# Optimization experiments

Measured on AMD Instinct MI355X. Metric: run time of the kernel, lower is better.

Reference implementation:

```python
import jax, jax.numpy as jnp
import numpy as np

N_NODES = 100000


def gcn_conv(x, W, b, row, col, ew, n_nodes):
    """PyG GCNConv: add self-loops (weight 1), symmetric normalization,
    out[c] = sum_{(r,c) in E} norm * (x @ W)[r] + b."""
    sl = jnp.arange(n_nodes, dtype=row.dtype)
    row2 = jnp.concatenate([row, sl])
    col2 = jnp.concatenate([col, sl])
    ew2 = jnp.concatenate([ew, jnp.ones((n_nodes,), dtype=ew.dtype)])
    deg = jax.ops.segment_sum(ew2, col2, num_segments=n_nodes)  # [N]
    dinv = jnp.where(deg > 0, jax.lax.rsqrt(jnp.where(deg > 0, deg, 1.0)), 0.0)
    norm = dinv[row2] * ew2 * dinv[col2]                         # [E+N]
    h = x @ W                                                    # [N, out]
    msg = h[row2] * norm[:, None]                                # gather + scale
    out = jax.ops.segment_sum(msg, col2, num_segments=n_nodes)   # scatter-add
    return out + b


def setup_inputs() -> dict:
    key = jax.random.key(0)
    k1, k2, k3, k4, k5 = jax.random.split(key, 5)
    F_IN, HID, C = 512, 16, 40
    E = 3200000
    x = jax.random.normal(k1, (N_NODES, F_IN), dtype=jnp.float32)
    edge_index = jax.random.randint(k2, (2, E), 0, N_NODES, dtype=jnp.int64)
    edge_weight = jax.random.uniform(k3, (E,), dtype=jnp.float32)
    # Glorot-ish init for weights
    W1 = jax.random.normal(k4, (F_IN, HID), dtype=jnp.float32) / np.sqrt(F_IN)
    b1 = jnp.zeros((HID,), dtype=jnp.float32)
    W2 = jax.random.normal(k5, (HID, C), dtype=jnp.float32) / np.sqrt(HID)
    b2 = jnp.zeros((C,), dtype=jnp.float32)
    return {"x": x, "edge_index": edge_index, "edge_weight": edge_weight,
            "W1": W1, "b1": b1, "W2": W2, "b2": b2}


def reference(x, edge_index, edge_weight, W1, b1, W2, b2):
    row, col = edge_index[0], edge_index[1]
    h = jax.nn.relu(gcn_conv(x, W1, b1, row, col, edge_weight, N_NODES))
    # dropout p=0.1 is identity at inference; DFALayer/DFA are identity in forward
    logits = gcn_conv(h, W2, b2, row, col, edge_weight, N_NODES)
    return jax.nn.log_softmax(logits, axis=1)
```

## Files before the change

kernel.cpp:

```cpp
#include <hip/hip_runtime.h>
#include <hip/hip_bf16.h>
#include <math.h>

#define F_IN 512
#define HID  16
#define C_OUT 40

#define BSH    7
#define BNODES 128
#define MAXNB  1024

#define EPB 8192
#define CTH 512

__device__ __forceinline__ unsigned short f2bf(float f) {
    unsigned u = __float_as_uint(f);
    unsigned r = (u + 0x7FFF + ((u >> 16) & 1)) >> 16;
    return (unsigned short)r;
}
__device__ __forceinline__ float bf2f(unsigned short h) {
    return __uint_as_float(((unsigned)h) << 16);
}

__global__ __launch_bounds__(1024) void k_zero(int* __restrict__ g, int n) {
    int t = threadIdx.x;
    if (t < n) g[t] = 0;
}

__global__ __launch_bounds__(CTH) void k_count(const int* __restrict__ col,
                                               int* __restrict__ gcnt,
                                               int E, int NB) {
    __shared__ int lc[MAXNB];
    int t = threadIdx.x;
    for (int i = t; i < NB; i += CTH) lc[i] = 0;
    __syncthreads();
    int base = blockIdx.x * EPB;
#pragma unroll
    for (int i = 0; i < EPB / CTH; ++i) {
        int e = base + t + i * CTH;
        if (e < E) atomicAdd(&lc[col[e] >> BSH], 1);
    }
    __syncthreads();
    for (int i = t; i < NB; i += CTH)
        if (lc[i]) atomicAdd(&gcnt[i], lc[i]);
}

__global__ __launch_bounds__(1024) void k_scan(const int* __restrict__ gcnt,
                                               int* __restrict__ bo,
                                               int* __restrict__ bcur,
                                               int* __restrict__ offs,
                                               int NB, int N, int E) {
    __shared__ int s[1024];
    int t = threadIdx.x;
    int v = (t < NB) ? gcnt[t] : 0;
    s[t] = v;
    __syncthreads();
    for (int off = 1; off < 1024; off <<= 1) {
        int x = (t >= off) ? s[t - off] : 0;
        __syncthreads();
        s[t] += x;
        __syncthreads();
    }
    if (t < NB) { int o = s[t] - v; bo[t] = o; bcur[t] = o; }
    if (t == 0) { bo[NB] = E; offs[N] = E; }
}

__global__ __launch_bounds__(CTH) void k_part(const int* __restrict__ row,
                                              const int* __restrict__ col,
                                              const float* __restrict__ ew,
                                              int* __restrict__ bcur,
                                              int2* __restrict__ st,
                                              int E, int NB) {
    __shared__ int lc[MAXNB];
    __shared__ int lb[MAXNB];
    int t = threadIdx.x;
    for (int i = t; i < NB; i += CTH) lc[i] = 0;
    __syncthreads();
    int base = blockIdx.x * EPB;
#pragma unroll
    for (int i = 0; i < EPB / CTH; ++i) {
        int e = base + t + i * CTH;
        if (e < E) atomicAdd(&lc[col[e] >> BSH], 1);
    }
    __syncthreads();
    for (int i = t; i < NB; i += CTH) {
        int c = lc[i];
        lb[i] = c ? atomicAdd(&bcur[i], c) : 0;
    }
    __syncthreads();
    for (int i = t; i < NB; i += CTH) lc[i] = 0;
    __syncthreads();
#pragma unroll
    for (int i = 0; i < EPB / CTH; ++i) {
        int e = base + t + i * CTH;
        if (e < E) {
            int c = col[e];
            int b = c >> BSH;
            int r = atomicAdd(&lc[b], 1);
            st[lb[b] + r] = make_int2((row[e] << BSH) | (c & (BNODES - 1)),
                                      __float_as_int(ew[e]));
        }
    }
}

__global__ __launch_bounds__(256) void k_sort(const int* __restrict__ bo,
                                              const int2* __restrict__ st,
                                              int2* __restrict__ st2,
                                              int* __restrict__ offs,
                                              float* __restrict__ dinv, int N) {
    __shared__ int cnt[BNODES];
    __shared__ float wsum[BNODES];
    __shared__ int off[BNODES];
    int t = threadIdx.x;
    int b = blockIdx.x;
    if (t < BNODES) { cnt[t] = 0; wsum[t] = 0.0f; }
    __syncthreads();
    int beg = bo[b], end = bo[b + 1];
    for (int e = beg + t; e < end; e += 256) {
        int2 rec = st[e];
        int cl = rec.x & (BNODES - 1);
        atomicAdd(&cnt[cl], 1);
        atomicAdd(&wsum[cl], __int_as_float(rec.y));
    }
    __syncthreads();
    if (t < BNODES) off[t] = cnt[t];
    __syncthreads();
    for (int o = 1; o < BNODES; o <<= 1) {
        int v = (t < BNODES && t >= o) ? off[t - o] : 0;
        __syncthreads();
        if (t < BNODES) off[t] += v;
        __syncthreads();
    }
    if (t < BNODES) {
        int ex = off[t] - cnt[t];
        off[t] = ex;
        int n = b * BNODES + t;
        if (n < N) {
            offs[n] = beg + ex;
            dinv[n] = rsqrtf(1.0f + wsum[t]);
        }
        cnt[t] = 0;
    }
    __syncthreads();
    for (int e = beg + t; e < end; e += 256) {
        int2 rec = st[e];
        int cl = rec.x & (BNODES - 1);
        int r = atomicAdd(&cnt[cl], 1);
        st2[beg + off[cl] + r] = make_int2(rec.x >> BSH, rec.y);
    }
}

__global__ __launch_bounds__(256) void k_gemm1(const float* __restrict__ x,
                                               const float* __restrict__ W,
                                               const float* __restrict__ dinv,
                                               unsigned short* __restrict__ hb,
                                               int N) {
    int n = blockIdx.x * 256 + threadIdx.x;
    if (n >= N) return;
    float acc[HID];
#pragma unroll
    for (int j = 0; j < HID; ++j) acc[j] = 0.0f;
    const float4* xr = (const float4*)(x + (size_t)n * F_IN);
#pragma unroll 4
    for (int k4 = 0; k4 < F_IN / 4; ++k4) {
        float4 xv = xr[k4];
        const float* wk = W + k4 * 4 * HID;
#pragma unroll
        for (int j = 0; j < HID; ++j) acc[j] += xv.x * wk[j];
#pragma unroll
        for (int j = 0; j < HID; ++j) acc[j] += xv.y * wk[HID + j];
#pragma unroll
        for (int j = 0; j < HID; ++j) acc[j] += xv.z * wk[2 * HID + j];
#pragma unroll
        for (int j = 0; j < HID; ++j) acc[j] += xv.w * wk[3 * HID + j];
    }
    float d = dinv[n];
    unsigned pk[8];
#pragma unroll
    for (int j = 0; j < 8; ++j)
        pk[j] = (unsigned)f2bf(d * acc[2 * j]) |
                ((unsigned)f2bf(d * acc[2 * j + 1]) << 16);
    uint4* hp = (uint4*)(hb + (size_t)n * HID);
    hp[0] = make_uint4(pk[0], pk[1], pk[2], pk[3]);
    hp[1] = make_uint4(pk[4], pk[5], pk[6], pk[7]);
}

__global__ __launch_bounds__(256) void k_agg1(const int* __restrict__ offs,
                                              const int2* __restrict__ st2,
                                              const float* __restrict__ dinv,
                                              const unsigned short* __restrict__ srcb,
                                              const float* __restrict__ bias,
                                              unsigned short* __restrict__ dstb,
                                              int N) {
    int t = threadIdx.x;
    int lane = t & 63, w = t >> 6;
    int n = blockIdx.x * 4 + w;
    if (n >= N) return;
    int q = lane & 3, i = lane >> 2;
    int beg = offs[n], end = offs[n + 1];
    float4 acc = make_float4(0.f, 0.f, 0.f, 0.f);
    for (int e = beg + i; e < end; e += 16) {
        int2 rec = st2[e];
        float wt = __int_as_float(rec.y);
        ushort4 v = ((const ushort4*)(srcb + (size_t)rec.x * HID))[q];
        acc.x += wt * bf2f(v.x);
        acc.y += wt * bf2f(v.y);
        acc.z += wt * bf2f(v.z);
        acc.w += wt * bf2f(v.w);
    }
#pragma unroll
    for (int off = 4; off < 64; off <<= 1) {
        acc.x += __shfl_xor(acc.x, off, 64);
        acc.y += __shfl_xor(acc.y, off, 64);
        acc.z += __shfl_xor(acc.z, off, 64);
        acc.w += __shfl_xor(acc.w, off, 64);
    }
    if (i == 0) {
        float d = dinv[n];
        ushort4 sv = ((const ushort4*)(srcb + (size_t)n * HID))[q];
        float4 bq = ((const float4*)bias)[q];
        float r0 = d * fmaxf(d * (acc.x + bf2f(sv.x)) + bq.x, 0.f);
        float r1 = d * fmaxf(d * (acc.y + bf2f(sv.y)) + bq.y, 0.f);
        float r2 = d * fmaxf(d * (acc.z + bf2f(sv.z)) + bq.z, 0.f);
        float r3 = d * fmaxf(d * (acc.w + bf2f(sv.w)) + bq.w, 0.f);
        ((ushort4*)(dstb + (size_t)n * HID))[q] =
            make_ushort4(f2bf(r0), f2bf(r1), f2bf(r2), f2bf(r3));
    }
}

__global__ __launch_bounds__(256) void k_agg2(const int* __restrict__ offs,
                                              const int2* __restrict__ st2,
                                              const float* __restrict__ dinv,
                                              const unsigned short* __restrict__ srcb,
                                              const float* __restrict__ W2,
                                              const float* __restrict__ b2,
                                              float* __restrict__ out, int N) {
    __shared__ float Ws[HID * C_OUT];
    __shared__ float bs[C_OUT];
    int t = threadIdx.x;
    for (int iw = t; iw < HID * C_OUT; iw += 256) Ws[iw] = W2[iw];
    if (t < C_OUT) bs[t] = b2[t];
    __syncthreads();

    int lane = t & 63, w = t >> 6;
    int n = blockIdx.x * 4 + w;
    if (n >= N) return;
    int q = lane & 3, i = lane >> 2;
    int beg = offs[n], end = offs[n + 1];
    float4 acc = make_float4(0.f, 0.f, 0.f, 0.f);
    for (int e = beg + i; e < end; e += 16) {
        int2 rec = st2[e];
        float wt = __int_as_float(rec.y);
        ushort4 v = ((const ushort4*)(srcb + (size_t)rec.x * HID))[q];
        acc.x += wt * bf2f(v.x);
        acc.y += wt * bf2f(v.y);
        acc.z += wt * bf2f(v.z);
        acc.w += wt * bf2f(v.w);
    }
#pragma unroll
    for (int off = 4; off < 64; off <<= 1) {
        acc.x += __shfl_xor(acc.x, off, 64);
        acc.y += __shfl_xor(acc.y, off, 64);
        acc.z += __shfl_xor(acc.z, off, 64);
        acc.w += __shfl_xor(acc.w, off, 64);
    }
    float d = dinv[n];
    ushort4 sv = ((const ushort4*)(srcb + (size_t)n * HID))[q];
    float gq[4];
    gq[0] = d * (acc.x + bf2f(sv.x));
    gq[1] = d * (acc.y + bf2f(sv.y));
    gq[2] = d * (acc.z + bf2f(sv.z));
    gq[3] = d * (acc.w + bf2f(sv.w));
    float g16[16];
    int base = lane & ~3;
#pragma unroll
    for (int qq = 0; qq < 4; ++qq) {
#pragma unroll
        for (int k = 0; k < 4; ++k)
            g16[qq * 4 + k] = __shfl(gq[k], base + qq, 64);
    }
    float logit = -INFINITY;
    if (lane < C_OUT) {
        float a = bs[lane];
#pragma unroll
        for (int j = 0; j < HID; ++j) a += g16[j] * Ws[j * C_OUT + lane];
        logit = a;
    }
    float m = logit;
#pragma unroll
    for (int off = 32; off > 0; off >>= 1) m = fmaxf(m, __shfl_xor(m, off, 64));
    float ex = (lane < C_OUT) ? __expf(logit - m) : 0.0f;
    float s = ex;
#pragma unroll
    for (int off = 32; off > 0; off >>= 1) s += __shfl_xor(s, off, 64);
    if (lane < C_OUT) out[(size_t)n * C_OUT + lane] = logit - m - __logf(s);
}

extern "C" void kernel_launch(void* const* d_in, const int* in_sizes, int n_in,
                              void* d_out, int out_size, void* d_ws, size_t ws_size,
                              hipStream_t stream) {
    const float* x   = (const float*)d_in[0];
    const int*   ei  = (const int*)d_in[1];
    const float* ew  = (const float*)d_in[2];
    const float* W1  = (const float*)d_in[3];
    const float* b1  = (const float*)d_in[4];
    const float* W2  = (const float*)d_in[5];
    const float* b2  = (const float*)d_in[6];
    float* out = (float*)d_out;

    const int N = in_sizes[0] / F_IN;
    const int E = in_sizes[2];
    const int* row = ei;
    const int* col = ei + E;
    const int NB = (N + BNODES - 1) >> BSH;

    int* wsi = (int*)d_ws;
    size_t o = 0;
    int* gcnt  = wsi + o; o += MAXNB;
    int* bo    = wsi + o; o += MAXNB + 1;
    int* bcur  = wsi + o; o += MAXNB;
    int* offs  = wsi + o; o += (size_t)N + 8;
    float* dinv = (float*)(wsi + o); o += N;
    unsigned short* h1b = (unsigned short*)(wsi + o); o += (size_t)N * HID / 2;
    unsigned short* a1b = (unsigned short*)(wsi + o); o += (size_t)N * HID / 2;
    int2* st   = (int2*)(wsi + o); o += (size_t)E * 2;
    int2* st2  = (int2*)(wsi + o); o += (size_t)E * 2;

    int gC = (E + EPB - 1) / EPB;
    int gW = (N + 3) / 4;

    k_zero<<<1, 1024, 0, stream>>>(gcnt, NB);
    k_count<<<gC, CTH, 0, stream>>>(col, gcnt, E, NB);
    k_scan<<<1, 1024, 0, stream>>>(gcnt, bo, bcur, offs, NB, N, E);
    k_part<<<gC, CTH, 0, stream>>>(row, col, ew, bcur, st, E, NB);
    k_sort<<<NB, 256, 0, stream>>>(bo, st, st2, offs, dinv, N);
    k_gemm1<<<(N + 255) / 256, 256, 0, stream>>>(x, W1, dinv, h1b, N);
    k_agg1<<<gW, 256, 0, stream>>>(offs, st2, dinv, h1b, b1, a1b, N);
    k_agg2<<<gW, 256, 0, stream>>>(offs, st2, dinv, a1b, W2, b2, out, N);
}
```

Before: 629.8 us.

## Stage x tiles into LDS via async global_load_lds with double buffering in gemm1

The first GEMM kernel no longer has each thread read its own 2KB row of x with strided float4 loads. It now cooperatively streams 32-column tiles of 256 rows into LDS using the direct global-to-LDS load builtin, with two buffers and an XOR swizzle to avoid bank conflicts. The aim is coalesced global reads of x (about 200MB, which dominates this kernel) and overlap of the next tile's load with the FMA work. The cost is 64KB of LDS per block, which limits occupancy, plus a barrier per tile.

```diff
diff --git a/kernel.cpp b/kernel.cpp
--- a/kernel.cpp
+++ b/kernel.cpp
@@ -12,6 +12,9 @@
 
 #define EPB 8192
 #define CTH 512
+
+#define GTK 32
+#define GTILES (F_IN / GTK)
 
 __device__ __forceinline__ unsigned short f2bf(float f) {
     unsigned u = __float_as_uint(f);
@@ -20,6 +23,12 @@
 }
 __device__ __forceinline__ float bf2f(unsigned short h) {
     return __uint_as_float(((unsigned)h) << 16);
+}
+
+__device__ __forceinline__ void gll16(const float* gp, void* lp) {
+    __builtin_amdgcn_global_load_lds(
+        (const __attribute__((address_space(1))) void*)gp,
+        (__attribute__((address_space(3))) void*)lp, 16, 0, 0);
 }
 
 __global__ __launch_bounds__(1024) void k_zero(int* __restrict__ g, int n) {
@@ -155,25 +164,58 @@
                                                const float* __restrict__ dinv,
                                                unsigned short* __restrict__ hb,
                                                int N) {
-    int n = blockIdx.x * 256 + threadIdx.x;
+    __shared__ float4 xt[2][256][8];
+
+    const int t = threadIdx.x;
+    const int lane = t & 63;
+    const int w = t >> 6;
+    const int lr = lane >> 3;
+    const int sc = (lane & 7) ^ lr;
+    const int n0 = blockIdx.x * 256;
+
+#define STAGE(kt, b)                                                        \
+    {                                                                       \
+        _Pragma("unroll")                                                   \
+        for (int it = 0; it < 8; ++it) {                                    \
+            int q  = w * 8 + it;              \
+            int rr = n0 + q * 8 + lr;                                       \
+            if (rr >= N) rr = N - 1;                                        \
+            const float* gp = x + (size_t)rr * F_IN + (kt) * GTK + sc * 4;  \
+            gll16(gp, (void*)&xt[b][q * 8][0]);                             \
+        }                                                                   \
+    }
+
+    float acc[HID];
+#pragma unroll
+    for (int j = 0; j < HID; ++j) acc[j] = 0.0f;
+
+    STAGE(0, 0);
+    __syncthreads();
+
+    const int sw = t & 7;
+    for (int kt = 0; kt < GTILES; ++kt) {
+        int b = kt & 1;
+        if (kt + 1 < GTILES) STAGE(kt + 1, b ^ 1);
+        const float4* xrow = &xt[b][t][0];
+#pragma unroll
+        for (int c = 0; c < 8; ++c) {
+            float4 xv = xrow[c ^ sw];
+            const float* wk = W + ((kt * GTK) + c * 4) * HID;
+#pragma unroll
+            for (int j = 0; j < HID; ++j) acc[j] += xv.x * wk[j];
+#pragma unroll
+            for (int j = 0; j < HID; ++j) acc[j] += xv.y * wk[HID + j];
+#pragma unroll
+            for (int j = 0; j < HID; ++j) acc[j] += xv.z * wk[2 * HID + j];
+#pragma unroll
+            for (int j = 0; j < HID; ++j) acc[j] += xv.w * wk[3 * HID + j];
+        }
+        __syncthreads();
+    }
+#undef STAGE
+
+    int n = n0 + t;
     if (n >= N) return;
-    float acc[HID];
-#pragma unroll
-    for (int j = 0; j < HID; ++j) acc[j] = 0.0f;
-    const float4* xr = (const float4*)(x + (size_t)n * F_IN);
-#pragma unroll 4
-    for (int k4 = 0; k4 < F_IN / 4; ++k4) {
-        float4 xv = xr[k4];
-        const float* wk = W + k4 * 4 * HID;
-#pragma unroll
-        for (int j = 0; j < HID; ++j) acc[j] += xv.x * wk[j];
-#pragma unroll
-        for (int j = 0; j < HID; ++j) acc[j] += xv.y * wk[HID + j];
-#pragma unroll
-        for (int j = 0; j < HID; ++j) acc[j] += xv.z * wk[2 * HID + j];
-#pragma unroll
-        for (int j = 0; j < HID; ++j) acc[j] += xv.w * wk[3 * HID + j];
-    }
     float d = dinv[n];
     unsigned pk[8];
 #pragma unroll
```

New measurement: 677.1 us. 7.5% more time.

## Restructure x@W1 GEMM to wave-per-row-block with coalesced loads and shuffle reduction

Applied to the files above, without the earlier changes.

The first-layer GEMM previously had each thread compute one full row, so each thread read a 2KB row with a large stride across the wave. Now each wave processes 16 rows: every lane holds a slice of W1 in registers, reads a coalesced float4 pair of each x row, prefetches the next row, and reduces the 16 outputs across lanes with a butterfly transpose-reduce via xor shuffles. This targets the uncoalesced, bandwidth-heavy x reads (about 200MB) at the cost of heavy register use (launch bounds 256,1), many shuffles per row, and fewer blocks in flight.

```diff
diff --git a/kernel.cpp b/kernel.cpp
--- a/kernel.cpp
+++ b/kernel.cpp
@@ -150,39 +150,115 @@
     }
 }
 
-__global__ __launch_bounds__(256) void k_gemm1(const float* __restrict__ x,
-                                               const float* __restrict__ W,
-                                               const float* __restrict__ dinv,
-                                               unsigned short* __restrict__ hb,
-                                               int N) {
-    int n = blockIdx.x * 256 + threadIdx.x;
-    if (n >= N) return;
-    float acc[HID];
-#pragma unroll
-    for (int j = 0; j < HID; ++j) acc[j] = 0.0f;
-    const float4* xr = (const float4*)(x + (size_t)n * F_IN);
-#pragma unroll 4
-    for (int k4 = 0; k4 < F_IN / 4; ++k4) {
-        float4 xv = xr[k4];
-        const float* wk = W + k4 * 4 * HID;
-#pragma unroll
-        for (int j = 0; j < HID; ++j) acc[j] += xv.x * wk[j];
-#pragma unroll
-        for (int j = 0; j < HID; ++j) acc[j] += xv.y * wk[HID + j];
-#pragma unroll
-        for (int j = 0; j < HID; ++j) acc[j] += xv.z * wk[2 * HID + j];
-#pragma unroll
-        for (int j = 0; j < HID; ++j) acc[j] += xv.w * wk[3 * HID + j];
-    }
-    float d = dinv[n];
-    unsigned pk[8];
-#pragma unroll
-    for (int j = 0; j < 8; ++j)
-        pk[j] = (unsigned)f2bf(d * acc[2 * j]) |
-                ((unsigned)f2bf(d * acc[2 * j + 1]) << 16);
-    uint4* hp = (uint4*)(hb + (size_t)n * HID);
-    hp[0] = make_uint4(pk[0], pk[1], pk[2], pk[3]);
-    hp[1] = make_uint4(pk[4], pk[5], pk[6], pk[7]);
+#define ROWS_PER_WAVE 16
+
+__global__ __launch_bounds__(256, 1) void k_gemm1(const float* __restrict__ x,
+                                                  const float* __restrict__ W,
+                                                  const float* __restrict__ dinv,
+                                                  unsigned short* __restrict__ hb,
+                                                  int N) {
+    const int t = threadIdx.x;
+    const int lane = t & 63;
+    const int wv = blockIdx.x * 4 + (t >> 6);
+    const int r0 = wv * ROWS_PER_WAVE;
+    if (r0 >= N) return;
+    const int rend = (r0 + ROWS_PER_WAVE < N) ? r0 + ROWS_PER_WAVE : N;
+
+    float4 Wa[4][4], Wb[4][4];
+    const float4* W4 = (const float4*)W;
+#pragma unroll
+    for (int q = 0; q < 4; ++q)
+#pragma unroll
+        for (int j4 = 0; j4 < 4; ++j4) {
+            Wa[q][j4] = W4[(4 * lane + q) * 4 + j4];
+            Wb[q][j4] = W4[(256 + 4 * lane + q) * 4 + j4];
+        }
+
+    const float4* xb4 = (const float4*)x;
+    float4 pa = xb4[(size_t)r0 * 128 + lane];
+    float4 pb = xb4[(size_t)r0 * 128 + 64 + lane];
+
+    for (int r = r0; r < rend; ++r) {
+        float4 ca = pa, cb = pb;
+        if (r + 1 < rend) {
+            pa = xb4[(size_t)(r + 1) * 128 + lane];
+            pb = xb4[(size_t)(r + 1) * 128 + 64 + lane];
+        }
+        float acc[16];
+#pragma unroll
+        for (int j = 0; j < 16; ++j) acc[j] = 0.0f;
+        const float xs0[4] = {ca.x, ca.y, ca.z, ca.w};
+        const float xs1[4] = {cb.x, cb.y, cb.z, cb.w};
+#pragma unroll
+        for (int q = 0; q < 4; ++q) {
+#pragma unroll
+            for (int j4 = 0; j4 < 4; ++j4) {
+                acc[j4 * 4 + 0] += xs0[q] * Wa[q][j4].x;
+                acc[j4 * 4 + 1] += xs0[q] * Wa[q][j4].y;
+                acc[j4 * 4 + 2] += xs0[q] * Wa[q][j4].z;
+                acc[j4 * 4 + 3] += xs0[q] * Wa[q][j4].w;
+            }
+        }
+#pragma unroll
+        for (int q = 0; q < 4; ++q) {
+#pragma unroll
+            for (int j4 = 0; j4 < 4; ++j4) {
+                acc[j4 * 4 + 0] += xs1[q] * Wb[q][j4].x;
+                acc[j4 * 4 + 1] += xs1[q] * Wb[q][j4].y;
+                acc[j4 * 4 + 2] += xs1[q] * Wb[q][j4].z;
+                acc[j4 * 4 + 3] += xs1[q] * Wb[q][j4].w;
+            }
+        }
+
+        const int b0 = lane & 1;
+        float v8[8];
+#pragma unroll
+        for (int m = 0; m < 8; ++m) {
+            float lo = acc[m], hi = acc[m + 8];
+            float sent = b0 ? lo : hi;
+            float recv = __shfl_xor(sent, 1, 64);
+            float keep = b0 ? hi : lo;
+            v8[m] = keep + recv;
+        }
+        const int b1 = (lane >> 1) & 1;
+        float v4[4];
+#pragma unroll
+        for (int m = 0; m < 4; ++m) {
+            float lo = v8[m], hi = v8[m + 4];
+            float sent = b1 ? lo : hi;
+            float recv = __shfl_xor(sent, 2, 64);
+            float keep = b1 ? hi : lo;
+            v4[m] = keep + recv;
+        }
+        const int b2 = (lane >> 2) & 1;
+        float v2[2];
+#pragma unroll
+        for (int m = 0; m < 2; ++m) {
+            float lo = v4[m], hi = v4[m + 2];
+            float sent = b2 ? lo : hi;
+            float recv = __shfl_xor(sent, 4, 64);
+            float keep = b2 ? hi : lo;
+            v2[m] = keep + recv;
+        }
+        const int b3 = (lane >> 3) & 1;
+        float v1;
+        {
+            float lo = v2[0], hi = v2[1];
+            float sent = b3 ? lo : hi;
+            float recv = __shfl_xor(sent, 8, 64);
+            float keep = b3 ? hi : lo;
+            v1 = keep + recv;
+        }
+        v1 += __shfl_xor(v1, 16, 64);
+        v1 += __shfl_xor(v1, 32, 64);
+
+        float d = dinv[r];
+        if (lane < 16) {
+            int j = ((lane & 1) << 3) | (((lane >> 1) & 1) << 2) |
+                    (((lane >> 2) & 1) << 1) | ((lane >> 3) & 1);
+            hb[(size_t)r * HID + j] = f2bf(d * v1);
+        }
+    }
 }
 
 __global__ __launch_bounds__(256) void k_agg1(const int* __restrict__ offs,
@@ -328,13 +404,14 @@
 
     int gC = (E + EPB - 1) / EPB;
     int gW = (N + 3) / 4;
+    int gG = (N + 4 * ROWS_PER_WAVE - 1) / (4 * ROWS_PER_WAVE);
 
     k_zero<<<1, 1024, 0, stream>>>(gcnt, NB);
     k_count<<<gC, CTH, 0, stream>>>(col, gcnt, E, NB);
     k_scan<<<1, 1024, 0, stream>>>(gcnt, bo, bcur, offs, NB, N, E);
     k_part<<<gC, CTH, 0, stream>>>(row, col, ew, bcur, st, E, NB);
     k_sort<<<NB, 256, 0, stream>>>(bo, st, st2, offs, dinv, N);
-    k_gemm1<<<(N + 255) / 256, 256, 0, stream>>>(x, W1, dinv, h1b, N);
+    k_gemm1<<<gG, 256, 0, stream>>>(x, W1, dinv, h1b, N);
     k_agg1<<<gW, 256, 0, stream>>>(offs, st2, dinv, h1b, b1, a1b, N);
     k_agg2<<<gW, 256, 0, stream>>>(offs, st2, dinv, a1b, W2, b2, out, N);
 }
```

After: 594.2 us. 1.06x faster.
